# Kernel optimization log

Hardware: AMD Instinct MI355X
Metric: run time of the kernel (lower is better)

## Reference

```python
import jax, jax.numpy as jnp
import numpy as np

B, N, NQ, D, H = 16, 1024, 1024, 512, 8
HD = D // H  # per-head kq dim and per-head v-output dim (64)


def setup_inputs() -> dict:
    key = jax.random.key(0)
    ks = jax.random.split(key, 7)
    s = 0.02  # small init like torch Linear default scale
    return {
        "x":   jax.random.normal(ks[0], (B, N, D), jnp.float32),
        "r":   jax.random.normal(ks[1], (B, N, D), jnp.float32),
        "x_q": jax.random.normal(ks[2], (B, NQ, D), jnp.float32),
        # per-head projection weights, torch Linear layout (out, in), stacked over heads
        "Wq": jax.random.normal(ks[3], (H, HD, D), jnp.float32) * s,
        "Wk": jax.random.normal(ks[4], (H, HD, D), jnp.float32) * s,
        "Wv": jax.random.normal(ks[5], (H, HD, D), jnp.float32) * s,  # applied AFTER attention
        "Wo": jax.random.normal(ks[6], (D, D), jnp.float32) * s,
    }


def reference(x, r, x_q, Wq, Wk, Wv, Wo):
    # AttentionAggregator.forward(x, r, x_q) -> MultiHeadAttention(q=x_q, k=x, v=r)
    qh = jnp.einsum('bnd,hed->bhne', x_q, Wq)            # (B,H,NQ,HD)
    kh = jnp.einsum('bmd,hed->bhme', x, Wk)              # (B,H,N,HD)
    scale = jnp.sqrt(jnp.float32(HD))                    # sqrt(d_k) with d_k = head_kq_dim_out
    scores = jnp.einsum('bhne,bhme->bhnm', qh, kh) / scale
    attn = jax.nn.softmax(scores, axis=-1)               # normalize=True path
    # NOTE: v (=r) is NOT projected before attention in the original module
    ctx = jnp.einsum('bhnm,bmd->bhnd', attn, r)          # (B,H,NQ,D)
    heads = jnp.einsum('bhnd,hed->bhne', ctx, Wv)        # (B,H,NQ,HD), per-head post-projection
    concat = heads.transpose(0, 2, 1, 3).reshape(B, NQ, H * HD)  # cat over heads, dim=-1
    return concat @ Wo.T                                 # head_o (post_process=True)
```

## Files before the change

### kernel.cpp

```cpp
#include <hip/hip_runtime.h>


#define B_  16
#define N_  1024
#define D_  512
#define M_  (B_ * N_)

typedef short short8 __attribute__((ext_vector_type(8)));
typedef float f32x4 __attribute__((ext_vector_type(4)));
typedef unsigned short ushort;
typedef unsigned int uint;

__device__ __forceinline__ ushort bf16rne(float f) {
  uint u = __float_as_uint(f);
  u += 0x7FFFu + ((u >> 16) & 1u);
  return (ushort)(u >> 16);
}
__device__ __forceinline__ uint bf16pk(float lo, float hi) {
  return (uint)bf16rne(lo) | ((uint)bf16rne(hi) << 16);
}
__device__ __forceinline__ void gload_lds16(const void* g, void* l) {
  __builtin_amdgcn_global_load_lds(
      (const __attribute__((address_space(1))) uint*)g,
      (__attribute__((address_space(3))) uint*)l, 16, 0, 0);
}
__device__ __forceinline__ float exp2_hw(float x) {
  float r;
  asm("v_exp_f32 %0, %1" : "=v"(r) : "v"(x));
  return r;
}
__device__ __forceinline__ uint cvtpk_bf16(float lo, float hi) {
  uint r;
  asm("v_cvt_pk_bf16_f32 %0, %1, %2" : "=v"(r) : "v"(lo), "v"(hi));
  return r;
}

union U4S8 { uint u[4]; short8 s; };

__global__ __launch_bounds__(256) void castW_k(
    const float* __restrict__ w0, const float* __restrict__ w1,
    const float* __restrict__ w2, const float* __restrict__ w3,
    ushort* __restrict__ d, long n)
{
  const int z = blockIdx.y;
  const float* s = (z == 0) ? w0 : (z == 1) ? w1 : (z == 2) ? w2 : w3;
  const float sc = (z == 0) ? 0.1803368801f : 1.f;
  ushort* dz = d + (long)z * n;
  long i = ((long)blockIdx.x * 256 + threadIdx.x) * 8;
  float4 v0 = *(const float4*)(s + i);
  float4 v1 = *(const float4*)(s + i + 4);
  uint4 o;
  o.x = bf16pk(v0.x * sc, v0.y * sc); o.y = bf16pk(v0.z * sc, v0.w * sc);
  o.z = bf16pk(v1.x * sc, v1.y * sc); o.w = bf16pk(v1.z * sc, v1.w * sc);
  *(uint4*)(dz + i) = o;
}

template <int MODE>
__global__ __launch_bounds__(256) void gemm_k(
    const float* __restrict__ Af0, const float* __restrict__ Af1,
    const float* __restrict__ Af2, const ushort* __restrict__ Abf,
    const ushort* __restrict__ Wbase, void* __restrict__ C0,
    ushort* __restrict__ Vt)
{
  const long SB = (long)M_ * D_, WB = (long)D_ * D_;
  const int nwg = gridDim.x, per = nwg >> 3;
  const int wg = ((int)blockIdx.x & 7) * per + ((int)blockIdx.x >> 3);
  int z, bx, by;
  if constexpr (MODE == 0) { z = wg >> 9; bx = wg & 3; by = (wg & 511) >> 2; }
  else                     { z = 0;       bx = wg & 3; by = wg >> 2; }
  const ushort* W = (MODE == 0) ? Wbase + z * WB : Wbase;

  __shared__ __align__(16) ushort Al[2][128 * 64];
  __shared__ __align__(16) ushort Bl[2][128 * 64];
  const int t = threadIdx.x, lane = t & 63, w = t >> 6;
  const int g = lane >> 4, lr = lane & 15;
  const int wr = w >> 1, wc = w & 1;
  const long m0 = (long)by * 128, n0 = (long)bx * 128;

  f32x4 acc[4][4] = {};

  auto LOADW = [&](int k0, int bufi) {
    #pragma unroll
    for (int u = 0; u < 4; ++u) {
      const int a = t * 16 + u * 4096;
      const int row = a >> 7, ch = (a >> 4) & 7;
      const int kk = k0 + ((ch ^ (row & 7)) << 3);
      gload_lds16(W + (n0 + row) * D_ + kk, (char*)Bl[bufi] + a);
    }
  };

  auto COMPUTE = [&](int cur) {
    short8 af[4][2], bf[4][2];
    #pragma unroll
    for (int mf = 0; mf < 4; ++mf)
      #pragma unroll
      for (int ks = 0; ks < 2; ++ks) {
        int row = wr * 64 + mf * 16 + lr;
        af[mf][ks] = *(const short8*)((const char*)Al[cur] + row * 128 + (((ks * 4 + g) ^ (row & 7)) << 4));
        row = wc * 64 + mf * 16 + lr;
        bf[mf][ks] = *(const short8*)((const char*)Bl[cur] + row * 128 + (((ks * 4 + g) ^ (row & 7)) << 4));
      }
    #pragma unroll
    for (int mf = 0; mf < 4; ++mf)
      #pragma unroll
      for (int nf = 0; nf < 4; ++nf)
        #pragma unroll
        for (int ks = 0; ks < 2; ++ks)
          acc[mf][nf] = __builtin_amdgcn_mfma_f32_16x16x32_bf16(
              af[mf][ks], bf[nf][ks], acc[mf][nf], 0, 0, 0);
  };

  if constexpr (MODE == 0) {
    const float* A = (z == 0) ? Af0 : (z == 1) ? Af1 : Af2;

    auto LOADA = [&](int k0, float4* rA) {
      #pragma unroll
      for (int u = 0; u < 4; ++u) {
        const int a = t * 16 + u * 4096;
        const int row = a >> 7, ch = (a >> 4) & 7;
        const float* src = A + (m0 + row) * D_ + k0 + ch * 8;
        rA[2 * u]     = *(const float4*)(src);
        rA[2 * u + 1] = *(const float4*)(src + 4);
      }
    };
    auto WRITEA = [&](const float4* rA, int bufi) {
      #pragma unroll
      for (int u = 0; u < 4; ++u) {
        const int a = t * 16 + u * 4096;
        const int row = a >> 7, ch = (a >> 4) & 7;
        const int dst = row * 128 + (((ch) ^ (row & 7)) << 4);
        uint4 o;
        o.x = cvtpk_bf16(rA[2 * u].x, rA[2 * u].y);
        o.y = cvtpk_bf16(rA[2 * u].z, rA[2 * u].w);
        o.z = cvtpk_bf16(rA[2 * u + 1].x, rA[2 * u + 1].y);
        o.w = cvtpk_bf16(rA[2 * u + 1].z, rA[2 * u + 1].w);
        *(uint4*)((char*)Al[bufi] + dst) = o;
      }
    };

    float4 rA0[8], rA1[8];
    LOADA(0, rA0);  LOADW(0, 0);
    LOADA(64, rA1); LOADW(64, 1);
    asm volatile("s_waitcnt vmcnt(12)" ::: "memory");
    WRITEA(rA0, 0);
    asm volatile("s_waitcnt lgkmcnt(0)" ::: "memory");
    __builtin_amdgcn_s_barrier();

    #pragma unroll
    for (int it = 0; it < 8; ++it) {
      const int cur = it & 1;
      COMPUTE(cur);
      asm volatile("s_waitcnt lgkmcnt(0)" ::: "memory");
      __builtin_amdgcn_s_barrier();
      if (it + 2 < 8) { LOADA((it + 2) * 64, cur ? rA1 : rA0); LOADW((it + 2) * 64, cur); }
      if (it + 1 < 8) {
        if (it + 2 < 8) asm volatile("s_waitcnt vmcnt(12)" ::: "memory");
        else            asm volatile("s_waitcnt vmcnt(0)"  ::: "memory");
        WRITEA(cur ? rA0 : rA1, cur ^ 1);
        asm volatile("s_waitcnt lgkmcnt(0)" ::: "memory");
        __builtin_amdgcn_s_barrier();
      }
    }
  } else {
    const ushort* A = Abf;
    auto STAGE = [&](int k0, int bufi) {
      #pragma unroll
      for (int u = 0; u < 4; ++u) {
        const int a = t * 16 + u * 4096;
        const int row = a >> 7, ch = (a >> 4) & 7;
        const int kk = k0 + ((ch ^ (row & 7)) << 3);
        gload_lds16(A + (m0 + row) * D_ + kk, (char*)Al[bufi] + a);
        gload_lds16(W + (n0 + row) * D_ + kk, (char*)Bl[bufi] + a);
      }
    };
    STAGE(0, 0);
    STAGE(64, 1);
    #pragma unroll
    for (int it = 0; it < 8; ++it) {
      const int cur = it & 1;
      if (it < 7) asm volatile("s_waitcnt vmcnt(8)" ::: "memory");
      else        asm volatile("s_waitcnt vmcnt(0)" ::: "memory");
      __builtin_amdgcn_s_barrier();
      COMPUTE(cur);
      asm volatile("s_waitcnt lgkmcnt(0)" ::: "memory");
      __builtin_amdgcn_s_barrier();
      if (it < 6) STAGE((it + 2) * 64, cur);
    }
  }

  if constexpr (MODE == 1) {
    float* C = (float*)C0;
    #pragma unroll
    for (int mf = 0; mf < 4; ++mf)
      #pragma unroll
      for (int nf = 0; nf < 4; ++nf)
        #pragma unroll
        for (int r = 0; r < 4; ++r)
          C[(m0 + wr * 64 + mf * 16 + g * 4 + r) * D_ + n0 + wc * 64 + nf * 16 + lr] =
              acc[mf][nf][r];
  } else {
    if (z < 2) {
      ushort* C = (ushort*)C0 + z * SB;
      #pragma unroll
      for (int mf = 0; mf < 4; ++mf)
        #pragma unroll
        for (int nf = 0; nf < 4; ++nf)
          #pragma unroll
          for (int r = 0; r < 4; ++r)
            C[(m0 + wr * 64 + mf * 16 + g * 4 + r) * D_ + n0 + wc * 64 + nf * 16 + lr] =
                bf16rne(acc[mf][nf][r]);
    } else {
      const int hh = (int)(n0 >> 6) + wc;
      #pragma unroll
      for (int mf = 0; mf < 4; ++mf) {
        const long m = m0 + wr * 64 + mf * 16 + g * 4;
        const int bb = (int)(m >> 10);
        const int kv = (int)(m & 1023);
        #pragma unroll
        for (int nf = 0; nf < 4; ++nf) {
          const int c = nf * 16 + lr;
          uint2 o2;
          o2.x = cvtpk_bf16(acc[mf][nf][0], acc[mf][nf][1]);
          o2.y = cvtpk_bf16(acc[mf][nf][2], acc[mf][nf][3]);
          *(uint2*)&Vt[((long)(bb * 8 + hh) * 64 + c) * (long)N_ + kv] = o2;
        }
      }
    }
  }
}

__global__ __launch_bounds__(256) void attn_mfma(
    const ushort* __restrict__ Q, const ushort* __restrict__ K,
    const ushort* __restrict__ Vt, ushort* __restrict__ Hd)
{
  __shared__ __align__(16) ushort Kl[2][64 * 64];
  __shared__ __align__(16) ushort Vl[2][64 * 64];
  const int t = threadIdx.x, lane = t & 63, w = t >> 6;
  const int g = lane >> 4, lr = lane & 15;
  const int bid = blockIdx.x;
  const int z = bid & 127, b = z >> 3, h = z & 7;
  const int qbase = (bid >> 7) * 128 + w * 32;

  short8 qf[2][2];
  #pragma unroll
  for (int nf = 0; nf < 2; ++nf)
    #pragma unroll
    for (int ks = 0; ks < 2; ++ks)
      qf[nf][ks] = *(const short8*)(Q + (long)(b * N_ + qbase + nf * 16 + lr) * D_ + h * 64 + ks * 32 + g * 8);

  const short8 ones = {0x3F80, 0x3F80, 0x3F80, 0x3F80, 0x3F80, 0x3F80, 0x3F80, 0x3F80};

  f32x4 o[2][4] = {};
  f32x4 acc_l[2] = {};

  const ushort* Kz = K + (long)b * N_ * D_ + h * 64;
  const ushort* Vz = Vt + (long)z * 64 * N_;

  auto STAGE = [&](int kt, int bufi) {
    #pragma unroll
    for (int u = 0; u < 2; ++u) {
      const int a = t * 16 + u * 4096;
      const int row = a >> 7, ch = (a >> 4) & 7;
      const int cc = (ch ^ (row & 7)) << 3;
      gload_lds16(Kz + (long)(kt * 64 + row) * D_ + cc, (char*)Kl[bufi] + a);
      gload_lds16(Vz + (long)row * N_ + kt * 64 + cc, (char*)Vl[bufi] + a);
    }
  };

  STAGE(0, 0);
  __syncthreads();

  for (int kt = 0; kt < 16; ++kt) {
    const int cur = kt & 1;
    if (kt < 15) STAGE(kt + 1, cur ^ 1);

    f32x4 s[4][2] = {};
    __builtin_amdgcn_s_setprio(1);
    #pragma unroll
    for (int mf = 0; mf < 4; ++mf) {
      short8 kf[2];
      #pragma unroll
      for (int ks = 0; ks < 2; ++ks) {
        const int row = mf * 16 + lr;
        kf[ks] = *(const short8*)((const char*)Kl[cur] + row * 128 + (((ks * 4 + g) ^ (row & 7)) << 4));
      }
      #pragma unroll
      for (int nf = 0; nf < 2; ++nf)
        #pragma unroll
        for (int ks = 0; ks < 2; ++ks)
          s[mf][nf] = __builtin_amdgcn_mfma_f32_16x16x32_bf16(kf[ks], qf[nf][ks], s[mf][nf], 0, 0, 0);
    }
    __builtin_amdgcn_s_setprio(0);

    short8 pa[2][2];
    #pragma unroll
    for (int nf = 0; nf < 2; ++nf) {
      uint Apk[4], Bpk[4];
      #pragma unroll
      for (int mf = 0; mf < 4; ++mf) {
        const float e0 = exp2_hw(s[mf][nf][0]);
        const float e1 = exp2_hw(s[mf][nf][1]);
        const float e2 = exp2_hw(s[mf][nf][2]);
        const float e3 = exp2_hw(s[mf][nf][3]);
        Apk[mf] = cvtpk_bf16(e0, e1);
        Bpk[mf] = cvtpk_bf16(e2, e3);
      }
      asm("v_permlane32_swap_b32 %0, %1" : "+v"(Apk[0]), "+v"(Apk[1]));
      asm("v_permlane16_swap_b32 %0, %1" : "+v"(Apk[0]), "+v"(Apk[1]));
      asm("v_permlane32_swap_b32 %0, %1" : "+v"(Bpk[0]), "+v"(Bpk[1]));
      asm("v_permlane16_swap_b32 %0, %1" : "+v"(Bpk[0]), "+v"(Bpk[1]));
      asm("v_permlane32_swap_b32 %0, %1" : "+v"(Apk[2]), "+v"(Apk[3]));
      asm("v_permlane16_swap_b32 %0, %1" : "+v"(Apk[2]), "+v"(Apk[3]));
      asm("v_permlane32_swap_b32 %0, %1" : "+v"(Bpk[2]), "+v"(Bpk[3]));
      asm("v_permlane16_swap_b32 %0, %1" : "+v"(Bpk[2]), "+v"(Bpk[3]));
      U4S8 u0, u1;
      u0.u[0] = Apk[0]; u0.u[1] = Bpk[0]; u0.u[2] = Apk[1]; u0.u[3] = Bpk[1];
      u1.u[0] = Apk[2]; u1.u[1] = Bpk[2]; u1.u[2] = Apk[3]; u1.u[3] = Bpk[3];
      pa[nf][0] = u0.s;
      pa[nf][1] = u1.s;
    }

    __builtin_amdgcn_s_setprio(1);
    #pragma unroll
    for (int ks = 0; ks < 2; ++ks) {
      short8 vb[4];
      #pragma unroll
      for (int nf = 0; nf < 4; ++nf) {
        const int row = nf * 16 + lr;
        vb[nf] = *(const short8*)((const char*)Vl[cur] + row * 128 + (((ks * 4 + g) ^ (row & 7)) << 4));
      }
      #pragma unroll
      for (int mf = 0; mf < 2; ++mf) {
        #pragma unroll
        for (int nf = 0; nf < 4; ++nf)
          o[mf][nf] = __builtin_amdgcn_mfma_f32_16x16x32_bf16(pa[mf][ks], vb[nf], o[mf][nf], 0, 0, 0);
        acc_l[mf] = __builtin_amdgcn_mfma_f32_16x16x32_bf16(pa[mf][ks], ones, acc_l[mf], 0, 0, 0);
      }
    }
    __builtin_amdgcn_s_setprio(0);
    __syncthreads();
  }

  #pragma unroll
  for (int mf = 0; mf < 2; ++mf)
    #pragma unroll
    for (int r = 0; r < 4; ++r) {
      const float inv = 1.f / acc_l[mf][r];
      const long grow = (long)b * N_ + qbase + mf * 16 + g * 4 + r;
      #pragma unroll
      for (int nf = 0; nf < 4; ++nf)
        Hd[grow * D_ + h * 64 + nf * 16 + lr] = bf16rne(o[mf][nf][r] * inv);
    }
}

extern "C" void kernel_launch(void* const* d_in, const int* in_sizes, int n_in,
                              void* d_out, int out_size, void* d_ws, size_t ws_size,
                              hipStream_t stream) {
  const float* x   = (const float*)d_in[0];
  const float* r   = (const float*)d_in[1];
  const float* x_q = (const float*)d_in[2];
  const float* Wq  = (const float*)d_in[3];
  const float* Wk  = (const float*)d_in[4];
  const float* Wv  = (const float*)d_in[5];
  const float* Wo  = (const float*)d_in[6];

  const long SBe = (long)M_ * D_;
  const long WBe = (long)D_ * D_;
  ushort* Qb  = (ushort*)d_ws;
  ushort* Kb  = Qb  + SBe;
  ushort* Vtb = Kb  + SBe;
  ushort* Hdb = Vtb + SBe;
  ushort* Wqb = Hdb + SBe;

  dim3 blk(256);
  castW_k<<<dim3(128, 4), blk, 0, stream>>>(Wq, Wk, Wv, Wo, Wqb, WBe);

  gemm_k<0><<<dim3(1536), blk, 0, stream>>>(x_q, x, r, nullptr, Wqb, Qb, Vtb);

  attn_mfma<<<dim3(1024), blk, 0, stream>>>(Qb, Kb, Vtb, Hdb);

  gemm_k<1><<<dim3(512), blk, 0, stream>>>(nullptr, nullptr, nullptr, Hdb,
                                           Wqb + 3 * WBe, d_out, nullptr);
}
```

Measured before the change: 241.7 us.

## Load fp32 A fragments directly into registers, bypassing LDS in projection GEMM

In the fp32-input projection GEMM, each wave now loads its own A rows straight from global memory in MFMA fragment layout and converts them to bf16 in registers. This removes the shared-memory staging of A and one barrier per k-step. Only the weights still go through LDS, and A is software-pipelined one step ahead. The cost is that A rows are loaded redundantly by the two column-waves (wc), plus higher register pressure from 16 float4 buffers.

```diff
diff --git a/kernel.cpp b/kernel.cpp
--- a/kernel.cpp
+++ b/kernel.cpp
@@ -70,7 +70,6 @@
   else                     { z = 0;       bx = wg & 3; by = wg >> 2; }
   const ushort* W = (MODE == 0) ? Wbase + z * WB : Wbase;
 
-  __shared__ __align__(16) ushort Al[2][128 * 64];
   __shared__ __align__(16) ushort Bl[2][128 * 64];
   const int t = threadIdx.x, lane = t & 63, w = t >> 6;
   const int g = lane >> 4, lr = lane & 15;
@@ -89,80 +88,77 @@
     }
   };
 
-  auto COMPUTE = [&](int cur) {
-    short8 af[4][2], bf[4][2];
-    #pragma unroll
-    for (int mf = 0; mf < 4; ++mf)
+  auto READB = [&](int cur, short8 (&bf)[4][2]) {
+    #pragma unroll
+    for (int nf = 0; nf < 4; ++nf)
       #pragma unroll
       for (int ks = 0; ks < 2; ++ks) {
-        int row = wr * 64 + mf * 16 + lr;
-        af[mf][ks] = *(const short8*)((const char*)Al[cur] + row * 128 + (((ks * 4 + g) ^ (row & 7)) << 4));
-        row = wc * 64 + mf * 16 + lr;
-        bf[mf][ks] = *(const short8*)((const char*)Bl[cur] + row * 128 + (((ks * 4 + g) ^ (row & 7)) << 4));
-      }
-    #pragma unroll
-    for (int mf = 0; mf < 4; ++mf)
-      #pragma unroll
-      for (int nf = 0; nf < 4; ++nf)
-        #pragma unroll
-        for (int ks = 0; ks < 2; ++ks)
-          acc[mf][nf] = __builtin_amdgcn_mfma_f32_16x16x32_bf16(
-              af[mf][ks], bf[nf][ks], acc[mf][nf], 0, 0, 0);
+        const int row = wc * 64 + nf * 16 + lr;
+        bf[nf][ks] = *(const short8*)((const char*)Bl[cur] + row * 128 + (((ks * 4 + g) ^ (row & 7)) << 4));
+      }
   };
 
   if constexpr (MODE == 0) {
     const float* A = (z == 0) ? Af0 : (z == 1) ? Af1 : Af2;
-
-    auto LOADA = [&](int k0, float4* rA) {
-      #pragma unroll
-      for (int u = 0; u < 4; ++u) {
-        const int a = t * 16 + u * 4096;
-        const int row = a >> 7, ch = (a >> 4) & 7;
-        const float* src = A + (m0 + row) * D_ + k0 + ch * 8;
-        rA[2 * u]     = *(const float4*)(src);
-        rA[2 * u + 1] = *(const float4*)(src + 4);
-      }
+    const float* Aw = A + (m0 + wr * 64 + lr) * D_;
+
+    float4 rA[16];
+    auto LOADA = [&](int k0) {
+      #pragma unroll
+      for (int mf = 0; mf < 4; ++mf)
+        #pragma unroll
+        for (int ks = 0; ks < 2; ++ks) {
+          const float* p = Aw + (long)mf * 16 * D_ + k0 + ks * 32 + g * 8;
+          rA[mf * 4 + ks * 2 + 0] = *(const float4*)p;
+          rA[mf * 4 + ks * 2 + 1] = *(const float4*)(p + 4);
+        }
     };
-    auto WRITEA = [&](const float4* rA, int bufi) {
-      #pragma unroll
-      for (int u = 0; u < 4; ++u) {
-        const int a = t * 16 + u * 4096;
-        const int row = a >> 7, ch = (a >> 4) & 7;
-        const int dst = row * 128 + (((ch) ^ (row & 7)) << 4);
-        uint4 o;
-        o.x = cvtpk_bf16(rA[2 * u].x, rA[2 * u].y);
-        o.y = cvtpk_bf16(rA[2 * u].z, rA[2 * u].w);
-        o.z = cvtpk_bf16(rA[2 * u + 1].x, rA[2 * u + 1].y);
-        o.w = cvtpk_bf16(rA[2 * u + 1].z, rA[2 * u + 1].w);
-        *(uint4*)((char*)Al[bufi] + dst) = o;
-      }
+    auto CVTA = [&](short8 (&af)[4][2]) {
+      #pragma unroll
+      for (int mf = 0; mf < 4; ++mf)
+        #pragma unroll
+        for (int ks = 0; ks < 2; ++ks) {
+          const float4 a0 = rA[mf * 4 + ks * 2 + 0];
+          const float4 a1 = rA[mf * 4 + ks * 2 + 1];
+          U4S8 u;
+          u.u[0] = cvtpk_bf16(a0.x, a0.y); u.u[1] = cvtpk_bf16(a0.z, a0.w);
+          u.u[2] = cvtpk_bf16(a1.x, a1.y); u.u[3] = cvtpk_bf16(a1.z, a1.w);
+          af[mf][ks] = u.s;
+        }
     };
 
-    float4 rA0[8], rA1[8];
-    LOADA(0, rA0);  LOADW(0, 0);
-    LOADA(64, rA1); LOADW(64, 1);
-    asm volatile("s_waitcnt vmcnt(12)" ::: "memory");
-    WRITEA(rA0, 0);
-    asm volatile("s_waitcnt lgkmcnt(0)" ::: "memory");
-    __builtin_amdgcn_s_barrier();
+    LOADA(0);
+    LOADW(0, 0);
+    LOADW(64, 1);
 
     #pragma unroll
     for (int it = 0; it < 8; ++it) {
       const int cur = it & 1;
-      COMPUTE(cur);
+      if (it < 7) asm volatile("s_waitcnt vmcnt(4)" ::: "memory");
+      else        asm volatile("s_waitcnt vmcnt(0)" ::: "memory");
+      __builtin_amdgcn_s_barrier();
+
+      short8 af[4][2], bf[4][2];
+      CVTA(af);
+      if (it + 1 < 8) LOADA((it + 1) * 64);
+      READB(cur, bf);
+
+      #pragma unroll
+      for (int mf = 0; mf < 4; ++mf)
+        #pragma unroll
+        for (int nf = 0; nf < 4; ++nf)
+          #pragma unroll
+          for (int ks = 0; ks < 2; ++ks)
+            acc[mf][nf] = __builtin_amdgcn_mfma_f32_16x16x32_bf16(
+                af[mf][ks], bf[nf][ks], acc[mf][nf], 0, 0, 0);
+
       asm volatile("s_waitcnt lgkmcnt(0)" ::: "memory");
       __builtin_amdgcn_s_barrier();
-      if (it + 2 < 8) { LOADA((it + 2) * 64, cur ? rA1 : rA0); LOADW((it + 2) * 64, cur); }
-      if (it + 1 < 8) {
-        if (it + 2 < 8) asm volatile("s_waitcnt vmcnt(12)" ::: "memory");
-        else            asm volatile("s_waitcnt vmcnt(0)"  ::: "memory");
-        WRITEA(cur ? rA0 : rA1, cur ^ 1);
-        asm volatile("s_waitcnt lgkmcnt(0)" ::: "memory");
-        __builtin_amdgcn_s_barrier();
-      }
+      if (it + 2 < 8) LOADW((it + 2) * 64, cur);
     }
   } else {
     const ushort* A = Abf;
+    __shared__ __align__(16) ushort Al[2][128 * 64];
     auto STAGE = [&](int k0, int bufi) {
       #pragma unroll
       for (int u = 0; u < 4; ++u) {
@@ -181,7 +177,23 @@
       if (it < 7) asm volatile("s_waitcnt vmcnt(8)" ::: "memory");
       else        asm volatile("s_waitcnt vmcnt(0)" ::: "memory");
       __builtin_amdgcn_s_barrier();
-      COMPUTE(cur);
+      short8 af[4][2], bf[4][2];
+      #pragma unroll
+      for (int mf = 0; mf < 4; ++mf)
+        #pragma unroll
+        for (int ks = 0; ks < 2; ++ks) {
+          const int row = wr * 64 + mf * 16 + lr;
+          af[mf][ks] = *(const short8*)((const char*)Al[cur] + row * 128 + (((ks * 4 + g) ^ (row & 7)) << 4));
+        }
+      READB(cur, bf);
+      #pragma unroll
+      for (int mf = 0; mf < 4; ++mf)
+        #pragma unroll
+        for (int nf = 0; nf < 4; ++nf)
+          #pragma unroll
+          for (int ks = 0; ks < 2; ++ks)
+            acc[mf][nf] = __builtin_amdgcn_mfma_f32_16x16x32_bf16(
+                af[mf][ks], bf[nf][ks], acc[mf][nf], 0, 0, 0);
       asm volatile("s_waitcnt lgkmcnt(0)" ::: "memory");
       __builtin_amdgcn_s_barrier();
       if (it < 6) STAGE((it + 2) * 64, cur);
```

After: 298.7 us. +23.6%, slower.
